# Kernel optimization log

Hardware: AMD Instinct MI355X
Metric: run time of the kernel (lower is better)

## Reference

```python
import jax, jax.numpy as jnp
import numpy as np

L, H = 16384, 1024

def setup_inputs() -> dict:
    key = jax.random.key(0)
    x = jax.random.normal(key, (L, H), dtype=jnp.float32)
    # learned parameter: tau initialized to log(0.8) per channel
    tau = jnp.full((H,), jnp.log(jnp.float32(0.8)), dtype=jnp.float32)
    return {"x": x, "tau": tau}

def _binop(q_i, q_j):
    # diagonal linear recurrence combine: x_j = A_j * x_i + b_j
    A_i, b_i = q_i
    A_j, b_j = q_j
    return (A_j * A_i, A_j * b_i + b_j)

def reference(x, tau):
    # Lambda_bar = exp(tau), B_bar = I  => Bu_elements = x
    Lambda_bar = jnp.exp(tau)                         # (H,)
    B_bar = jnp.eye(x.shape[1], dtype=x.dtype)        # (H, H) identity, as in original
    Bu = jnp.einsum('ph,lh->lp', B_bar, x)            # (L, H) == x
    Lambda_elements = jnp.broadcast_to(Lambda_bar, x.shape)  # (L, H)
    _, xs = jax.lax.associative_scan(_binop, (Lambda_elements, Bu))
    return xs  # (L, H)
```

## Files before the change

### kernel.cpp

```cpp
#include <hip/hip_runtime.h>
#include <hip/hip_cooperative_groups.h>
#include <cmath>


namespace cg = cooperative_groups;

static constexpr int TC = 16;
static constexpr int P  = 16;
static constexpr int FS = 32;

typedef float nt4 __attribute__((ext_vector_type(4)));

__device__ inline float4 ntload(const float4* p) {
    nt4 v = __builtin_nontemporal_load((const nt4*)p);
    return make_float4(v.x, v.y, v.z, v.w);
}

__device__ inline unsigned ld_flag(unsigned* p) {
    return __hip_atomic_load(p, __ATOMIC_RELAXED, __HIP_MEMORY_SCOPE_AGENT);
}
__device__ inline void st_flag(unsigned* p, unsigned v) {
    __hip_atomic_store(p, v, __ATOMIC_RELEASE, __HIP_MEMORY_SCOPE_AGENT);
}

__global__ __launch_bounds__(256, 4)
void li_lookback(const float4* __restrict__ xv, const float4* __restrict__ tauv,
                 float4* __restrict__ yv, float4* __restrict__ ends,
                 float4* __restrict__ pagg, float4* __restrict__ qc,
                 unsigned* __restrict__ eflag, unsigned* __restrict__ aflag,
                 unsigned* __restrict__ qflag, int HV)
{
    const int t = threadIdx.x;
    const int c = blockIdx.x;
    const int p = c / P;
    const int r = c % P;

    const float4 tv = tauv[t];
    const float lx = expf(tv.x), ly = expf(tv.y),
                lz = expf(tv.z), lw = expf(tv.w);
    const float Tx = expf(tv.x * (float)TC), Ty = expf(tv.y * (float)TC),
                Tz = expf(tv.z * (float)TC), Tw = expf(tv.w * (float)TC);

    const size_t base = (size_t)c * TC * HV + t;
    float4 buf[TC];
#pragma unroll
    for (int i = 0; i < TC; ++i)
        buf[i] = ntload(&xv[base + (size_t)i * HV]);

    float4 s = make_float4(0.f, 0.f, 0.f, 0.f);
#pragma unroll
    for (int i = 0; i < TC; ++i) {
        s.x = fmaf(lx, s.x, buf[i].x);
        s.y = fmaf(ly, s.y, buf[i].y);
        s.z = fmaf(lz, s.z, buf[i].z);
        s.w = fmaf(lw, s.w, buf[i].w);
        buf[i] = s;
    }
    ends[(size_t)c * HV + t] = s;
    __threadfence();
    __syncthreads();
    if (t == 0) st_flag(&eflag[(size_t)c * FS], 1u);

    if (t < r) {
        while (ld_flag(&eflag[(size_t)(p * P + t) * FS]) == 0u)
            __builtin_amdgcn_s_sleep(1);
    }
    __syncthreads();
    __threadfence();

    float4 w = make_float4(0.f, 0.f, 0.f, 0.f);
    const float4* ep = ends + (size_t)p * P * HV + t;
    for (int j0 = 0; j0 < r; j0 += 4) {
        float4 v[4];
#pragma unroll
        for (int j = 0; j < 4; ++j)
            if (j0 + j < r) v[j] = ep[(size_t)(j0 + j) * HV];
#pragma unroll
        for (int j = 0; j < 4; ++j) {
            if (j0 + j < r) {
                w.x = fmaf(Tx, w.x, v[j].x);
                w.y = fmaf(Ty, w.y, v[j].y);
                w.z = fmaf(Tz, w.z, v[j].z);
                w.w = fmaf(Tw, w.w, v[j].w);
            }
        }
    }

    float4 cc;
    const float fr = (float)(TC * r);
    if (r == P - 1) {
        float4 a;
        a.x = fmaf(Tx, w.x, s.x);
        a.y = fmaf(Ty, w.y, s.y);
        a.z = fmaf(Tz, w.z, s.z);
        a.w = fmaf(Tw, w.w, s.w);
        pagg[(size_t)p * HV + t] = a;
        __threadfence();
        __syncthreads();
        if (t == 0) st_flag(&aflag[(size_t)p * FS], 1u);

        if (t < p) {
            while (ld_flag(&aflag[(size_t)t * FS]) == 0u)
                __builtin_amdgcn_s_sleep(1);
        }
        __syncthreads();
        __threadfence();

        const float fQ = (float)(TC * P);
        const float Qx = expf(tv.x * fQ), Qy = expf(tv.y * fQ),
                    Qz = expf(tv.z * fQ), Qw = expf(tv.w * fQ);
        float4 carry = make_float4(0.f, 0.f, 0.f, 0.f);
        for (int q0 = 0; q0 < p; q0 += 4) {
            float4 v[4];
#pragma unroll
            for (int j = 0; j < 4; ++j)
                if (q0 + j < p) v[j] = pagg[(size_t)(q0 + j) * HV + t];
#pragma unroll
            for (int j = 0; j < 4; ++j) {
                if (q0 + j < p) {
                    carry.x = fmaf(Qx, carry.x, v[j].x);
                    carry.y = fmaf(Qy, carry.y, v[j].y);
                    carry.z = fmaf(Qz, carry.z, v[j].z);
                    carry.w = fmaf(Qw, carry.w, v[j].w);
                }
            }
        }
        qc[(size_t)p * HV + t] = carry;
        __threadfence();
        __syncthreads();
        if (t == 0) st_flag(&qflag[(size_t)p * FS], 1u);

        const float Rx = expf(tv.x * fr), Ry = expf(tv.y * fr),
                    Rz = expf(tv.z * fr), Rw = expf(tv.w * fr);
        cc.x = fmaf(Rx, carry.x, w.x);
        cc.y = fmaf(Ry, carry.y, w.y);
        cc.z = fmaf(Rz, carry.z, w.z);
        cc.w = fmaf(Rw, carry.w, w.w);
    } else {
        if (t == 0) {
            while (ld_flag(&qflag[(size_t)p * FS]) == 0u)
                __builtin_amdgcn_s_sleep(1);
        }
        __syncthreads();
        __threadfence();
        const float4 qv = qc[(size_t)p * HV + t];
        const float Rx = expf(tv.x * fr), Ry = expf(tv.y * fr),
                    Rz = expf(tv.z * fr), Rw = expf(tv.w * fr);
        cc.x = fmaf(Rx, qv.x, w.x);
        cc.y = fmaf(Ry, qv.y, w.y);
        cc.z = fmaf(Rz, qv.z, w.z);
        cc.w = fmaf(Rw, qv.w, w.w);
    }

    float4 pm = make_float4(lx, ly, lz, lw);
    nt4* yn = (nt4*)yv;
#pragma unroll
    for (int i = 0; i < TC; ++i) {
        nt4 o = { fmaf(pm.x, cc.x, buf[i].x),
                  fmaf(pm.y, cc.y, buf[i].y),
                  fmaf(pm.z, cc.z, buf[i].z),
                  fmaf(pm.w, cc.w, buf[i].w) };
        __builtin_nontemporal_store(o, &yn[base + (size_t)i * HV]);
        pm.x *= lx; pm.y *= ly; pm.z *= lz; pm.w *= lw;
    }
}


__global__ __launch_bounds__(256, 4)
void li_coop(const float4* __restrict__ xv, const float4* __restrict__ tauv,
             float4* __restrict__ yv, float4* __restrict__ ends,
             float4* __restrict__ pa, int HV, int NP)
{
    const int t = threadIdx.x;
    const int c = blockIdx.x;

    const float4 tv = tauv[t];
    const float lx = expf(tv.x), ly = expf(tv.y),
                lz = expf(tv.z), lw = expf(tv.w);
    const float Tx = expf(tv.x * (float)TC), Ty = expf(tv.y * (float)TC),
                Tz = expf(tv.z * (float)TC), Tw = expf(tv.w * (float)TC);
    const float fQ = (float)(TC * P);
    const float Qx = expf(tv.x * fQ), Qy = expf(tv.y * fQ),
                Qz = expf(tv.z * fQ), Qw = expf(tv.w * fQ);

    const size_t base = (size_t)c * TC * HV + t;
    float4 buf[TC];
#pragma unroll
    for (int i = 0; i < TC; ++i)
        buf[i] = ntload(&xv[base + (size_t)i * HV]);

    float4 s = make_float4(0.f, 0.f, 0.f, 0.f);
#pragma unroll
    for (int i = 0; i < TC; ++i) {
        s.x = fmaf(lx, s.x, buf[i].x);
        s.y = fmaf(ly, s.y, buf[i].y);
        s.z = fmaf(lz, s.z, buf[i].z);
        s.w = fmaf(lw, s.w, buf[i].w);
        buf[i] = s;
    }
    ends[(size_t)c * HV + t] = s;

    cg::this_grid().sync();

    if (c < NP) {
        const float4* ep = ends + (size_t)c * P * HV + t;
        float4 a = make_float4(0.f, 0.f, 0.f, 0.f);
#pragma unroll
        for (int j0 = 0; j0 < P; j0 += 8) {
            float4 v[8];
#pragma unroll
            for (int j = 0; j < 8; ++j)
                v[j] = ep[(size_t)(j0 + j) * HV];
#pragma unroll
            for (int j = 0; j < 8; ++j) {
                a.x = fmaf(Tx, a.x, v[j].x);
                a.y = fmaf(Ty, a.y, v[j].y);
                a.z = fmaf(Tz, a.z, v[j].z);
                a.w = fmaf(Tw, a.w, v[j].w);
            }
        }
        pa[(size_t)c * HV + t] = a;
    }

    cg::this_grid().sync();

    const int p = c / P;
    const int r = c % P;

    float4 carry = make_float4(0.f, 0.f, 0.f, 0.f);
    for (int q0 = 0; q0 < p; q0 += 8) {
        const int n = p - q0;
        float4 v[8];
#pragma unroll
        for (int j = 0; j < 8; ++j)
            if (j < n) v[j] = pa[(size_t)(q0 + j) * HV + t];
#pragma unroll
        for (int j = 0; j < 8; ++j) {
            if (j < n) {
                carry.x = fmaf(Qx, carry.x, v[j].x);
                carry.y = fmaf(Qy, carry.y, v[j].y);
                carry.z = fmaf(Qz, carry.z, v[j].z);
                carry.w = fmaf(Qw, carry.w, v[j].w);
            }
        }
    }
    {
        const float4* ep = ends + (size_t)p * P * HV + t;
        for (int j0 = 0; j0 < r; j0 += 8) {
            const int n = r - j0;
            float4 v[8];
#pragma unroll
            for (int j = 0; j < 8; ++j)
                if (j < n) v[j] = ep[(size_t)(j0 + j) * HV];
#pragma unroll
            for (int j = 0; j < 8; ++j) {
                if (j < n) {
                    carry.x = fmaf(Tx, carry.x, v[j].x);
                    carry.y = fmaf(Ty, carry.y, v[j].y);
                    carry.z = fmaf(Tz, carry.z, v[j].z);
                    carry.w = fmaf(Tw, carry.w, v[j].w);
                }
            }
        }
    }

    float4 pm = make_float4(lx, ly, lz, lw);
    nt4* yn = (nt4*)yv;
#pragma unroll
    for (int i = 0; i < TC; ++i) {
        nt4 o = { fmaf(pm.x, carry.x, buf[i].x),
                  fmaf(pm.y, carry.y, buf[i].y),
                  fmaf(pm.z, carry.z, buf[i].z),
                  fmaf(pm.w, carry.w, buf[i].w) };
        __builtin_nontemporal_store(o, &yn[base + (size_t)i * HV]);
        pm.x *= lx; pm.y *= ly; pm.z *= lz; pm.w *= lw;
    }
}


__global__ __launch_bounds__(256)
void li_ends(const float4* __restrict__ xv, const float4* __restrict__ tauv,
             float4* __restrict__ ends, int HV) {
    const int t = threadIdx.x;
    const int c = blockIdx.x;
    const float4 tv = tauv[t];
    const float lx = expf(tv.x), ly = expf(tv.y),
                lz = expf(tv.z), lw = expf(tv.w);
    const float4* xp = xv + (size_t)c * TC * HV + t;
    float4 buf[TC];
#pragma unroll
    for (int i = 0; i < TC; ++i)
        buf[i] = xp[(size_t)i * HV];
    float4 s = make_float4(0.f, 0.f, 0.f, 0.f);
#pragma unroll
    for (int i = 0; i < TC; ++i) {
        s.x = fmaf(lx, s.x, buf[i].x);
        s.y = fmaf(ly, s.y, buf[i].y);
        s.z = fmaf(lz, s.z, buf[i].z);
        s.w = fmaf(lw, s.w, buf[i].w);
    }
    ends[(size_t)c * HV + t] = s;
}

__global__ __launch_bounds__(256)
void li_pagg(const float4* __restrict__ ends, const float4* __restrict__ tauv,
             float4* __restrict__ pa, int HV) {
    const int gid = blockIdx.x * 256 + threadIdx.x;
    const int t = gid % HV;
    const int p = gid / HV;
    const float4 tv = tauv[t];
    const float Tx = expf(tv.x * (float)TC), Ty = expf(tv.y * (float)TC),
                Tz = expf(tv.z * (float)TC), Tw = expf(tv.w * (float)TC);
    const float4* ep = ends + (size_t)p * P * HV + t;
    float4 buf[P];
#pragma unroll
    for (int j = 0; j < P; ++j)
        buf[j] = ep[(size_t)j * HV];
    float4 s = make_float4(0.f, 0.f, 0.f, 0.f);
#pragma unroll
    for (int j = 0; j < P; ++j) {
        s.x = fmaf(Tx, s.x, buf[j].x);
        s.y = fmaf(Ty, s.y, buf[j].y);
        s.z = fmaf(Tz, s.z, buf[j].z);
        s.w = fmaf(Tw, s.w, buf[j].w);
    }
    pa[(size_t)p * HV + t] = s;
}

__global__ __launch_bounds__(256)
void li_pscan(float4* __restrict__ pa, const float4* __restrict__ tauv,
              int HV, int NP) {
    const int t = threadIdx.x;
    const float4 tv = tauv[t];
    const float fP = (float)(P * TC);
    const float Px = expf(tv.x * fP), Py = expf(tv.y * fP),
                Pz = expf(tv.z * fP), Pw = expf(tv.w * fP);
    float4 c = make_float4(0.f, 0.f, 0.f, 0.f);
    for (int p0 = 0; p0 < NP; p0 += 16) {
        float4 v[16];
#pragma unroll
        for (int j = 0; j < 16; ++j)
            v[j] = pa[(size_t)(p0 + j) * HV + t];
#pragma unroll
        for (int j = 0; j < 16; ++j) {
            const float4 a = v[j];
            v[j] = c;
            c.x = fmaf(Px, c.x, a.x);
            c.y = fmaf(Py, c.y, a.y);
            c.z = fmaf(Pz, c.z, a.z);
            c.w = fmaf(Pw, c.w, a.w);
        }
#pragma unroll
        for (int j = 0; j < 16; ++j)
            pa[(size_t)(p0 + j) * HV + t] = v[j];
    }
}

__global__ __launch_bounds__(256)
void li_out(const float4* __restrict__ xv, const float4* __restrict__ tauv,
            const float4* __restrict__ ends, const float4* __restrict__ pc,
            float4* __restrict__ yv, int HV) {
    const int t = threadIdx.x;
    const int c = blockIdx.x;
    const int p = c / P;
    const int r = c % P;
    const float4 tv = tauv[t];
    const float lx = expf(tv.x), ly = expf(tv.y),
                lz = expf(tv.z), lw = expf(tv.w);
    const float Tx = expf(tv.x * (float)TC), Ty = expf(tv.y * (float)TC),
                Tz = expf(tv.z * (float)TC), Tw = expf(tv.w * (float)TC);
    float4 carry = pc[(size_t)p * HV + t];
    {
        float4 v[P - 1];
        const float4* ep = ends + (size_t)p * P * HV + t;
#pragma unroll
        for (int j = 0; j < P - 1; ++j)
            if (j < r) v[j] = ep[(size_t)j * HV];
#pragma unroll
        for (int j = 0; j < P - 1; ++j) {
            if (j < r) {
                carry.x = fmaf(Tx, carry.x, v[j].x);
                carry.y = fmaf(Ty, carry.y, v[j].y);
                carry.z = fmaf(Tz, carry.z, v[j].z);
                carry.w = fmaf(Tw, carry.w, v[j].w);
            }
        }
    }
    const size_t base = (size_t)c * TC * HV + t;
    float4 buf[TC];
#pragma unroll
    for (int i = 0; i < TC; ++i)
        buf[i] = xv[base + (size_t)i * HV];
    float4 s = carry;
#pragma unroll
    for (int i = 0; i < TC; ++i) {
        s.x = fmaf(lx, s.x, buf[i].x);
        s.y = fmaf(ly, s.y, buf[i].y);
        s.z = fmaf(lz, s.z, buf[i].z);
        s.w = fmaf(lw, s.w, buf[i].w);
        buf[i] = s;
    }
    nt4* yn = (nt4*)yv;
#pragma unroll
    for (int i = 0; i < TC; ++i) {
        nt4 o = { buf[i].x, buf[i].y, buf[i].z, buf[i].w };
        __builtin_nontemporal_store(o, &yn[base + (size_t)i * HV]);
    }
}

extern "C" void kernel_launch(void* const* d_in, const int* in_sizes, int n_in,
                              void* d_out, int out_size, void* d_ws, size_t ws_size,
                              hipStream_t stream) {
    const float* x   = (const float*)d_in[0];
    const float* tau = (const float*)d_in[1];
    float* y = (float*)d_out;

    const int H  = in_sizes[1];
    const int L  = in_sizes[0] / H;
    const int C  = L / TC;
    const int NP = C / P;
    const int HV = H / 4;

    float4* ends = (float4*)d_ws;
    float4* pagg = ends + (size_t)C * HV;
    float4* qc   = pagg + (size_t)NP * HV;
    unsigned* eflag = (unsigned*)(qc + (size_t)NP * HV);
    unsigned* aflag = eflag + (size_t)C * FS;
    unsigned* qflag = aflag + (size_t)NP * FS;
    const size_t flagBytes = (size_t)(C + 2 * NP) * FS * sizeof(unsigned);
    const size_t needLB = ((size_t)C * HV + 2 * (size_t)NP * HV) * sizeof(float4)
                          + flagBytes;

    const float4* xv   = (const float4*)x;
    const float4* tauv = (const float4*)tau;
    float4*       yv   = (float4*)y;

    static int lb_bpc = -1;
    static int nCU    = -1;
    if (lb_bpc < 0) {
        int b = 0;
        if (hipOccupancyMaxActiveBlocksPerMultiprocessor(&b, li_lookback, 256, 0)
            != hipSuccess) b = 0;
        lb_bpc = b;
        hipDeviceProp_t prop;
        int dev = 0;
        if (hipGetDevice(&dev) == hipSuccess &&
            hipGetDeviceProperties(&prop, dev) == hipSuccess)
            nCU = prop.multiProcessorCount;
        else
            nCU = 0;
    }

    if (lb_bpc >= 4 && (size_t)lb_bpc * (size_t)nCU >= (size_t)C &&
        ws_size >= needLB) {
        hipMemsetAsync(eflag, 0, flagBytes, stream);
        li_lookback<<<dim3(C), dim3(256), 0, stream>>>(
            xv, tauv, yv, ends, pagg, qc, eflag, aflag, qflag, HV);
        return;
    }

    int blocksPerCU = 0;
    hipError_t qe = hipOccupancyMaxActiveBlocksPerMultiprocessor(
        &blocksPerCU, li_coop, 256, 0);
    bool coop_ok = false;
    if (qe == hipSuccess && blocksPerCU >= 4) {
        void* args[] = { (void*)&xv, (void*)&tauv, (void*)&yv,
                         (void*)&ends, (void*)&pagg, (void*)&HV, (void*)&NP };
        hipError_t le = hipLaunchCooperativeKernel(
            li_coop, dim3(C), dim3(256), args, 0u, stream);
        coop_ok = (le == hipSuccess);
    }

    if (!coop_ok) {
        li_ends <<<dim3(C),             dim3(256), 0, stream>>>(xv, tauv, ends, HV);
        li_pagg <<<dim3(NP * HV / 256), dim3(256), 0, stream>>>(ends, tauv, pagg, HV);
        li_pscan<<<dim3(1),             dim3(256), 0, stream>>>(pagg, tauv, HV, NP);
        li_out  <<<dim3(C),             dim3(256), 0, stream>>>(xv, tauv, ends, pagg,
                                                                yv, HV);
    }
}
```

Before: 132.7 us.

## Centralize per-partition carry computation in representative block and broadcast carries

Each partition's last block now waits for the chunk-end values of its peers, computes the partition aggregate and the cross-partition carry, then writes an individual carry for every chunk in the partition and signals each with its own flag. The other blocks only publish their chunk end and wait for that per-chunk carry. Before, every block reloaded its preceding peers' ends and waited on a shared partition flag. This cuts redundant lookback reads and exp computations but serializes the chunk carries through one block and adds a workspace buffer and flags. Input loads also switch from nontemporal to normal loads, and the sleep durations change.

```diff
diff --git a/kernel.cpp b/kernel.cpp
--- a/kernel.cpp
+++ b/kernel.cpp
@@ -24,11 +24,11 @@
 }
 
 __global__ __launch_bounds__(256, 4)
-void li_lookback(const float4* __restrict__ xv, const float4* __restrict__ tauv,
-                 float4* __restrict__ yv, float4* __restrict__ ends,
-                 float4* __restrict__ pagg, float4* __restrict__ qc,
-                 unsigned* __restrict__ eflag, unsigned* __restrict__ aflag,
-                 unsigned* __restrict__ qflag, int HV)
+void li_rep(const float4* __restrict__ xv, const float4* __restrict__ tauv,
+            float4* __restrict__ yv, float4* __restrict__ ends,
+            float4* __restrict__ pagg, float4* __restrict__ kc,
+            unsigned* __restrict__ eflag, unsigned* __restrict__ aflag,
+            unsigned* __restrict__ kflag, int HV)
 {
     const int t = threadIdx.x;
     const int c = blockIdx.x;
@@ -45,7 +45,7 @@
     float4 buf[TC];
 #pragma unroll
     for (int i = 0; i < TC; ++i)
-        buf[i] = ntload(&xv[base + (size_t)i * HV]);
+        buf[i] = xv[base + (size_t)i * HV];
 
     float4 s = make_float4(0.f, 0.f, 0.f, 0.f);
 #pragma unroll
@@ -56,44 +56,49 @@
         s.w = fmaf(lw, s.w, buf[i].w);
         buf[i] = s;
     }
-    ends[(size_t)c * HV + t] = s;
-    __threadfence();
-    __syncthreads();
-    if (t == 0) st_flag(&eflag[(size_t)c * FS], 1u);
-
-    if (t < r) {
-        while (ld_flag(&eflag[(size_t)(p * P + t) * FS]) == 0u)
-            __builtin_amdgcn_s_sleep(1);
-    }
-    __syncthreads();
-    __threadfence();
-
-    float4 w = make_float4(0.f, 0.f, 0.f, 0.f);
-    const float4* ep = ends + (size_t)p * P * HV + t;
-    for (int j0 = 0; j0 < r; j0 += 4) {
-        float4 v[4];
-#pragma unroll
-        for (int j = 0; j < 4; ++j)
-            if (j0 + j < r) v[j] = ep[(size_t)(j0 + j) * HV];
-#pragma unroll
-        for (int j = 0; j < 4; ++j) {
-            if (j0 + j < r) {
-                w.x = fmaf(Tx, w.x, v[j].x);
-                w.y = fmaf(Ty, w.y, v[j].y);
-                w.z = fmaf(Tz, w.z, v[j].z);
-                w.w = fmaf(Tw, w.w, v[j].w);
-            }
-        }
-    }
 
     float4 cc;
-    const float fr = (float)(TC * r);
-    if (r == P - 1) {
-        float4 a;
-        a.x = fmaf(Tx, w.x, s.x);
-        a.y = fmaf(Ty, w.y, s.y);
-        a.z = fmaf(Tz, w.z, s.z);
-        a.w = fmaf(Tw, w.w, s.w);
+    if (r != P - 1) {
+        ends[(size_t)c * HV + t] = s;
+        __threadfence();
+        __syncthreads();
+        if (t == 0) {
+            st_flag(&eflag[(size_t)c * FS], 1u);
+            while (ld_flag(&kflag[(size_t)c * FS]) == 0u)
+                __builtin_amdgcn_s_sleep(8);
+        }
+        __syncthreads();
+        __threadfence();
+        cc = kc[(size_t)c * HV + t];
+    } else {
+        if (t < P - 1) {
+            while (ld_flag(&eflag[(size_t)(c - (P - 1) + t) * FS]) == 0u)
+                __builtin_amdgcn_s_sleep(2);
+        }
+        __syncthreads();
+        __threadfence();
+
+        const float4* ep = ends + (size_t)p * P * HV + t;
+
+        float4 a = make_float4(0.f, 0.f, 0.f, 0.f);
+#pragma unroll
+        for (int j0 = 0; j0 < P - 1; j0 += 5) {
+            float4 v[5];
+#pragma unroll
+            for (int j = 0; j < 5; ++j)
+                v[j] = ep[(size_t)(j0 + j) * HV];
+#pragma unroll
+            for (int j = 0; j < 5; ++j) {
+                a.x = fmaf(Tx, a.x, v[j].x);
+                a.y = fmaf(Ty, a.y, v[j].y);
+                a.z = fmaf(Tz, a.z, v[j].z);
+                a.w = fmaf(Tw, a.w, v[j].w);
+            }
+        }
+        a.x = fmaf(Tx, a.x, s.x);
+        a.y = fmaf(Ty, a.y, s.y);
+        a.z = fmaf(Tz, a.z, s.z);
+        a.w = fmaf(Tw, a.w, s.w);
         pagg[(size_t)p * HV + t] = a;
         __threadfence();
         __syncthreads();
@@ -101,7 +106,7 @@
 
         if (t < p) {
             while (ld_flag(&aflag[(size_t)t * FS]) == 0u)
-                __builtin_amdgcn_s_sleep(1);
+                __builtin_amdgcn_s_sleep(2);
         }
         __syncthreads();
         __threadfence();
@@ -109,7 +114,7 @@
         const float fQ = (float)(TC * P);
         const float Qx = expf(tv.x * fQ), Qy = expf(tv.y * fQ),
                     Qz = expf(tv.z * fQ), Qw = expf(tv.w * fQ);
-        float4 carry = make_float4(0.f, 0.f, 0.f, 0.f);
+        float4 q = make_float4(0.f, 0.f, 0.f, 0.f);
         for (int q0 = 0; q0 < p; q0 += 4) {
             float4 v[4];
 #pragma unroll
@@ -118,38 +123,34 @@
 #pragma unroll
             for (int j = 0; j < 4; ++j) {
                 if (q0 + j < p) {
-                    carry.x = fmaf(Qx, carry.x, v[j].x);
-                    carry.y = fmaf(Qy, carry.y, v[j].y);
-                    carry.z = fmaf(Qz, carry.z, v[j].z);
-                    carry.w = fmaf(Qw, carry.w, v[j].w);
+                    q.x = fmaf(Qx, q.x, v[j].x);
+                    q.y = fmaf(Qy, q.y, v[j].y);
+                    q.z = fmaf(Qz, q.z, v[j].z);
+                    q.w = fmaf(Qw, q.w, v[j].w);
                 }
             }
         }
-        qc[(size_t)p * HV + t] = carry;
-        __threadfence();
-        __syncthreads();
-        if (t == 0) st_flag(&qflag[(size_t)p * FS], 1u);
-
-        const float Rx = expf(tv.x * fr), Ry = expf(tv.y * fr),
-                    Rz = expf(tv.z * fr), Rw = expf(tv.w * fr);
-        cc.x = fmaf(Rx, carry.x, w.x);
-        cc.y = fmaf(Ry, carry.y, w.y);
-        cc.z = fmaf(Rz, carry.z, w.z);
-        cc.w = fmaf(Rw, carry.w, w.w);
-    } else {
-        if (t == 0) {
-            while (ld_flag(&qflag[(size_t)p * FS]) == 0u)
-                __builtin_amdgcn_s_sleep(1);
-        }
-        __syncthreads();
-        __threadfence();
-        const float4 qv = qc[(size_t)p * HV + t];
-        const float Rx = expf(tv.x * fr), Ry = expf(tv.y * fr),
-                    Rz = expf(tv.z * fr), Rw = expf(tv.w * fr);
-        cc.x = fmaf(Rx, qv.x, w.x);
-        cc.y = fmaf(Ry, qv.y, w.y);
-        cc.z = fmaf(Rz, qv.z, w.z);
-        cc.w = fmaf(Rw, qv.w, w.w);
+
+        float4 k = q;
+#pragma unroll
+        for (int j0 = 0; j0 < P - 1; j0 += 5) {
+            float4 v[5];
+#pragma unroll
+            for (int j = 0; j < 5; ++j)
+                v[j] = ep[(size_t)(j0 + j) * HV];
+#pragma unroll
+            for (int j = 0; j < 5; ++j) {
+                kc[(size_t)(p * P + j0 + j) * HV + t] = k;
+                k.x = fmaf(Tx, k.x, v[j].x);
+                k.y = fmaf(Ty, k.y, v[j].y);
+                k.z = fmaf(Tz, k.z, v[j].z);
+                k.w = fmaf(Tw, k.w, v[j].w);
+            }
+        }
+        __threadfence();
+        __syncthreads();
+        if (t < P - 1) st_flag(&kflag[(size_t)(c - (P - 1) + t) * FS], 1u);
+        cc = k;
     }
 
     float4 pm = make_float4(lx, ly, lz, lw);
@@ -423,12 +424,12 @@
 
     float4* ends = (float4*)d_ws;
     float4* pagg = ends + (size_t)C * HV;
-    float4* qc   = pagg + (size_t)NP * HV;
-    unsigned* eflag = (unsigned*)(qc + (size_t)NP * HV);
+    float4* kc   = pagg + (size_t)NP * HV;
+    unsigned* eflag = (unsigned*)(kc + (size_t)C * HV);
     unsigned* aflag = eflag + (size_t)C * FS;
-    unsigned* qflag = aflag + (size_t)NP * FS;
-    const size_t flagBytes = (size_t)(C + 2 * NP) * FS * sizeof(unsigned);
-    const size_t needLB = ((size_t)C * HV + 2 * (size_t)NP * HV) * sizeof(float4)
+    unsigned* kflag = aflag + (size_t)NP * FS;
+    const size_t flagBytes = (size_t)(2 * C + NP) * FS * sizeof(unsigned);
+    const size_t needLB = ((size_t)2 * C * HV + (size_t)NP * HV) * sizeof(float4)
                           + flagBytes;
 
     const float4* xv   = (const float4*)x;
@@ -439,7 +440,7 @@
     static int nCU    = -1;
     if (lb_bpc < 0) {
         int b = 0;
-        if (hipOccupancyMaxActiveBlocksPerMultiprocessor(&b, li_lookback, 256, 0)
+        if (hipOccupancyMaxActiveBlocksPerMultiprocessor(&b, li_rep, 256, 0)
             != hipSuccess) b = 0;
         lb_bpc = b;
         hipDeviceProp_t prop;
@@ -454,8 +455,8 @@
     if (lb_bpc >= 4 && (size_t)lb_bpc * (size_t)nCU >= (size_t)C &&
         ws_size >= needLB) {
         hipMemsetAsync(eflag, 0, flagBytes, stream);
-        li_lookback<<<dim3(C), dim3(256), 0, stream>>>(
-            xv, tauv, yv, ends, pagg, qc, eflag, aflag, qflag, HV);
+        li_rep<<<dim3(C), dim3(256), 0, stream>>>(
+            xv, tauv, yv, ends, pagg, kc, eflag, aflag, kflag, HV);
         return;
     }
 
```

After: 132.1 us. Within noise of the previous version (-0.4%).
